# Kernel tuning notes

Measured on AMD Instinct MI355X. Metric: run time of the kernel, lower is better.

The kernel has to match this reference:

```python
import jax, jax.numpy as jnp
import numpy as np

B, H, W, C = 8, 64, 64, 256
CK = C // 8  # key/query dim of conv_f / conv_g


def setup_inputs() -> dict:
    key = jax.random.key(0)
    ks = jax.random.split(key, 10)
    s = lambda fan_in: 1.0 / np.sqrt(fan_in)
    return {
        "x": jax.random.normal(ks[0], (B, H, W, C), dtype=jnp.float32),
        "Wf": jax.random.normal(ks[1], (C, CK), dtype=jnp.float32) * s(C),
        "bf": jnp.zeros((CK,), dtype=jnp.float32),
        "Wg": jax.random.normal(ks[2], (C, CK), dtype=jnp.float32) * s(C),
        "bg": jnp.zeros((CK,), dtype=jnp.float32),
        "Wh": jax.random.normal(ks[3], (C, C), dtype=jnp.float32) * s(C),
        "bh": jnp.zeros((C,), dtype=jnp.float32),
        "Wo": jax.random.normal(ks[4], (C, C), dtype=jnp.float32) * s(C),
        "bo": jnp.zeros((C,), dtype=jnp.float32),
        # original init is zeros; use a random scalar so output/grads are nontrivial
        "gamma": jax.random.normal(ks[5], (1,), dtype=jnp.float32),
    }


def reference(x, Wf, bf, Wg, bg, Wh, bh, Wo, bo, gamma):
    b, h, w, c = x.shape
    n = h * w
    xf = x.reshape(b, n, c)                       # flatten spatial: [B, N, C]
    # 1x1 convs == per-pixel matmuls
    f = xf @ Wf + bf                              # [B, N, C//8]
    g = xf @ Wg + bg                              # [B, N, C//8]
    hh = xf @ Wh + bh                             # [B, N, C]
    # scores[b, i, j] = <g_i, f_j>; softmax over j (keys)
    scores = jnp.einsum("bnd,bmd->bnm", g, f)     # [B, N, N]
    attn = jax.nn.softmax(scores, axis=-1)
    o = jnp.einsum("bnm,bmc->bnc", attn, hh)      # [B, N, C]
    o = o @ Wo + bo                               # conv_o (1x1)
    out = gamma * o + xf                          # gamma residual
    return out.reshape(b, h, w, c)
```

## Files before the change

kernel.cpp:

```cpp
#include <hip/hip_runtime.h>
#include <hip/hip_fp16.h>
#include <hip/hip_bf16.h>

constexpr int BB  = 8;
constexpr int NN  = 4096;
constexpr int CC  = 256;
constexpr int CKK = 32;

typedef __attribute__((ext_vector_type(8))) short    short8;
typedef __attribute__((ext_vector_type(8))) _Float16 half8;
typedef __attribute__((ext_vector_type(4))) _Float16 half4;
typedef __attribute__((ext_vector_type(4))) float    f32x4;

__device__ __forceinline__ unsigned short bf16_bits(float v) {
    __hip_bfloat16 h = __float2bfloat16(v);
    return *reinterpret_cast<unsigned short*>(&h);
}
__device__ __forceinline__ float bf16_val(unsigned short u) {
    __hip_bfloat16 h = *reinterpret_cast<__hip_bfloat16*>(&u);
    return __bfloat162float(h);
}
__device__ __forceinline__ float exp2_x(float x) {
#if __has_builtin(__builtin_amdgcn_exp2f)
    return __builtin_amdgcn_exp2f(x);
#else
    return exp2f(x);
#endif
}

__global__ __launch_bounds__(256) void prep_kernel(
    const float* __restrict__ Wf, const float* __restrict__ Wg,
    const float* __restrict__ Wh, const float* __restrict__ Wo,
    unsigned short* __restrict__ WThi, unsigned short* __restrict__ WTlo)
{
    const int n = blockIdx.x;
    const int k = threadIdx.x;
    float v;
    if      (n < 256) v = Wh[k * 256 + n];
    else if (n < 288) v = Wf[k * 32 + (n - 256)];
    else if (n < 320) v = Wg[k * 32 + (n - 288)];
    else              v = Wo[k * 256 + (n - 320)];
    const unsigned short hi = bf16_bits(v);
    WThi[n * 256 + k] = hi;
    WTlo[n * 256 + k] = bf16_bits(v - bf16_val(hi));
}

__global__ __launch_bounds__(256) void fgh_kernel(
    const float* __restrict__ x,
    const unsigned short* __restrict__ WThi, const unsigned short* __restrict__ WTlo,
    const float* __restrict__ bf, const float* __restrict__ bg,
    const float* __restrict__ bh,
    _Float16* __restrict__ fbuf, _Float16* __restrict__ gbuf,
    _Float16* __restrict__ hhT)
{
    __shared__ __align__(16) float XT[2][64 * 36];

    const int tid = threadIdx.x, w = tid >> 6, lane = tid & 63;
    const int ln = lane & 15, lq = lane >> 4;
    const int b  = blockIdx.x & 7;
    const int q0 = (blockIdx.x >> 3) * 64;
    const size_t px0 = (size_t)b * NN + q0;
    const int n0 = w * 80;

    const int p  = tid >> 2;
    const int jq = tid & 3;
    const float* xrow = &x[(px0 + p) * CC + jq * 8];

    f32x4 acc[4][5];
    #pragma unroll
    for (int i = 0; i < 4; ++i)
        #pragma unroll
        for (int j = 0; j < 5; ++j) acc[i][j] = {0.f, 0.f, 0.f, 0.f};

    short8 Ahi[4], Alo[4];
    float4 ra0 = *(const float4*)&xrow[0];
    float4 ra1 = *(const float4*)&xrow[4];

    int cur = 0;
    #pragma unroll 1
    for (int kc = 0; kc < 8; ++kc) {
        const int k0 = kc * 32;
        float* dst = &XT[cur][p * 36 + jq * 8];
        *(float4*)&dst[0] = ra0;
        *(float4*)&dst[4] = ra1;
        __syncthreads();
        if (kc < 7) {
            ra0 = *(const float4*)&xrow[(kc + 1) * 32];
            ra1 = *(const float4*)&xrow[(kc + 1) * 32 + 4];
        }
        #pragma unroll
        for (int mt = 0; mt < 4; ++mt) {
            float av[8];
            const float* sp = &XT[cur][(mt * 16 + ln) * 36 + lq * 8];
            *(float4*)&av[0] = *(const float4*)&sp[0];
            *(float4*)&av[4] = *(const float4*)&sp[4];
            #pragma unroll
            for (int j = 0; j < 8; ++j) {
                const unsigned short h = bf16_bits(av[j]);
                Ahi[mt][j] = (short)h;
                Alo[mt][j] = (short)bf16_bits(av[j] - bf16_val(h));
            }
        }
        #pragma unroll
        for (int nt = 0; nt < 5; ++nt) {
            const size_t boff = (size_t)(n0 + nt * 16 + ln) * 256 + k0 + lq * 8;
            const short8 Bhi = *(const short8*)&WThi[boff];
            const short8 Blo = *(const short8*)&WTlo[boff];
            #pragma unroll
            for (int mt = 0; mt < 4; ++mt) {
                acc[mt][nt] = __builtin_amdgcn_mfma_f32_16x16x32_bf16(Ahi[mt], Bhi, acc[mt][nt], 0, 0, 0);
                acc[mt][nt] = __builtin_amdgcn_mfma_f32_16x16x32_bf16(Ahi[mt], Blo, acc[mt][nt], 0, 0, 0);
                acc[mt][nt] = __builtin_amdgcn_mfma_f32_16x16x32_bf16(Alo[mt], Bhi, acc[mt][nt], 0, 0, 0);
            }
        }
        cur ^= 1;
    }

    _Float16* st = (_Float16*)&XT[0][0] + w * 1088;
    const int rr = lane >> 3, k8 = lane & 7;

    #pragma unroll
    for (int nt = 0; nt < 5; ++nt) {
        const int cbase = n0 + nt * 16;
        const int c = cbase + ln;
        if (cbase < 256) {
            const float bias = bh[c];
            #pragma unroll
            for (int mt = 0; mt < 4; ++mt) {
                half4 hv;
                #pragma unroll
                for (int r = 0; r < 4; ++r) hv[r] = (_Float16)(acc[mt][nt][r] + bias);
                *(half4*)&st[ln * 68 + mt * 16 + lq * 4] = hv;
            }
            #pragma unroll
            for (int i = 0; i < 2; ++i) {
                const half8 row = *(const half8*)&st[(i * 8 + rr) * 68 + k8 * 8];
                *(half8*)&hhT[((size_t)(b * CC + cbase + i * 8 + rr)) * NN + q0 + k8 * 8] = row;
            }
        } else {
            const bool isf = (c < 288);
            const int d = isf ? (c - 256) : (c - 288);
            const float bias = isf ? bf[d] : bg[d];
            _Float16* dst2 = isf ? fbuf : gbuf;
            #pragma unroll
            for (int mt = 0; mt < 4; ++mt)
                #pragma unroll
                for (int r = 0; r < 4; ++r)
                    dst2[(px0 + mt * 16 + lq * 4 + r) * CKK + d] =
                        (_Float16)(acc[mt][nt][r] + bias);
        }
    }
}

__global__ __launch_bounds__(256) void rowmax_kernel(
    const _Float16* __restrict__ fbuf, const _Float16* __restrict__ gbuf,
    float* __restrict__ mxpart)
{
    __shared__ float mxbuf[4][64];

    const int tid = threadIdx.x, w = tid >> 6, lane = tid & 63;
    const int ln = lane & 15, lq = lane >> 4;
    const int b  = blockIdx.x & 7;
    const int q0 = (blockIdx.x >> 3) * 64;
    const int kp = blockIdx.y;

    const f32x4 zero = {0.f, 0.f, 0.f, 0.f};

    half8 Bg[4];
    #pragma unroll
    for (int qt = 0; qt < 4; ++qt)
        Bg[qt] = *(const half8*)&gbuf[(size_t)(b * NN + q0 + qt * 16 + ln) * CKK + lq * 8];

    const _Float16* fb = &fbuf[(size_t)(b * NN + kp * 1024 + w * 16 + ln) * CKK + lq * 8];

    float mx[4];
    #pragma unroll
    for (int qt = 0; qt < 4; ++qt) mx[qt] = -1e30f;
    half8 Afc = *(const half8*)fb;
    #pragma unroll 1
    for (int j0 = 0; j0 < 1024; j0 += 64) {
        const int jn = (j0 + 64 < 1024) ? j0 + 64 : j0;
        const half8 Afn = *(const half8*)&fb[(size_t)jn * CKK];
        #pragma unroll
        for (int qt = 0; qt < 4; ++qt) {
            const f32x4 s = __builtin_amdgcn_mfma_f32_16x16x32_f16(Afc, Bg[qt], zero, 0, 0, 0);
            mx[qt] = fmaxf(mx[qt], fmaxf(fmaxf(s[0], s[1]), fmaxf(s[2], s[3])));
        }
        Afc = Afn;
    }
    #pragma unroll
    for (int qt = 0; qt < 4; ++qt) {
        mx[qt] = fmaxf(mx[qt], __shfl_xor(mx[qt], 16));
        mx[qt] = fmaxf(mx[qt], __shfl_xor(mx[qt], 32));
    }
    if (lane < 16) {
        #pragma unroll
        for (int qt = 0; qt < 4; ++qt) mxbuf[w][qt * 16 + ln] = mx[qt];
    }
    __syncthreads();
    if (tid < 64) {
        const float m = fmaxf(fmaxf(mxbuf[0][tid], mxbuf[1][tid]),
                              fmaxf(mxbuf[2][tid], mxbuf[3][tid]));
        mxpart[(size_t)kp * (BB * NN) + (size_t)b * NN + q0 + tid] = m;
    }
}

__global__ __launch_bounds__(256, 2) void attn_kernel(
    const _Float16* __restrict__ fbuf, const _Float16* __restrict__ gbuf,
    const _Float16* __restrict__ hhT, const float* __restrict__ mxpart,
    const unsigned short* __restrict__ WThi, const unsigned short* __restrict__ WTlo,
    const float* __restrict__ bo, const float* __restrict__ gamma,
    const float* __restrict__ x, float* __restrict__ out)
{
    __shared__ __align__(16) float OF[64 * 268];
    _Float16* P0 = (_Float16*)OF;
    _Float16* P1 = P0 + 64 * 72;
    __shared__ float rsbuf[4][64];

    const int tid = threadIdx.x, w = tid >> 6, lane = tid & 63;
    const int ln = lane & 15, lq = lane >> 4;
    const int b  = blockIdx.x & 7;
    const int q0 = (blockIdx.x >> 3) * 64;
    const int cb = w * 64;

    const f32x4 zero = {0.f, 0.f, 0.f, 0.f};
    constexpr float LOG2E = 1.4426950408889634f;

    half8 Bg[4];
    #pragma unroll
    for (int qt = 0; qt < 4; ++qt)
        Bg[qt] = *(const half8*)&gbuf[(size_t)(b * NN + q0 + qt * 16 + ln) * CKK + lq * 8];

    const _Float16* fb = &fbuf[(size_t)(b * NN + w * 16 + ln) * CKK + lq * 8];
    const _Float16* hb = &hhT[((size_t)(b * CC + cb + ln)) * NN + lq * 8];

    float mk[4];
    #pragma unroll
    for (int qt = 0; qt < 4; ++qt) {
        const float* mp = &mxpart[(size_t)b * NN + q0 + qt * 16 + ln];
        const float m = fmaxf(fmaxf(mp[0], mp[BB * NN]),
                              fmaxf(mp[2 * (BB * NN)], mp[3 * (BB * NN)]));
        mk[qt] = LOG2E * m;
    }

    f32x4 O[4][4];
    #pragma unroll
    for (int qt = 0; qt < 4; ++qt)
        #pragma unroll
        for (int ct = 0; ct < 4; ++ct) O[qt][ct] = zero;
    float psum[4] = {0.f, 0.f, 0.f, 0.f};

    auto phaseA = [&](const half8& Af, _Float16* Pb) {
        #pragma unroll
        for (int qt = 0; qt < 4; ++qt) {
            const f32x4 s = __builtin_amdgcn_mfma_f32_16x16x32_f16(Af, Bg[qt], zero, 0, 0, 0);
            half4 ph;
            float ps = 0.f;
            #pragma unroll
            for (int r = 0; r < 4; ++r) {
                const float p = exp2_x(fmaf(s[r], LOG2E, -mk[qt]));
                ps += p;
                ph[r] = (_Float16)p;
            }
            psum[qt] += ps;
            *(half4*)&Pb[(qt * 16 + ln) * 72 + w * 16 + lq * 4] = ph;
        }
    };

    auto loadBh = [&](half8 (&Bh)[4][2], int j0) {
        #pragma unroll
        for (int ct = 0; ct < 4; ++ct)
            #pragma unroll
            for (int kh = 0; kh < 2; ++kh)
                Bh[ct][kh] = *(const half8*)&hb[(size_t)ct * 16 * NN + j0 + kh * 32];
    };

    auto phaseB = [&](const half8 (&Bh)[4][2], const _Float16* Pb) {
        __builtin_amdgcn_s_setprio(1);
        #pragma unroll
        for (int qt = 0; qt < 4; ++qt) {
            const half8 Ap0 = *(const half8*)&Pb[(qt * 16 + ln) * 72 + lq * 8];
            const half8 Ap1 = *(const half8*)&Pb[(qt * 16 + ln) * 72 + 32 + lq * 8];
            #pragma unroll
            for (int ct = 0; ct < 4; ++ct) {
                O[qt][ct] = __builtin_amdgcn_mfma_f32_16x16x32_f16(Ap0, Bh[ct][0], O[qt][ct], 0, 0, 0);
                O[qt][ct] = __builtin_amdgcn_mfma_f32_16x16x32_f16(Ap1, Bh[ct][1], O[qt][ct], 0, 0, 0);
            }
        }
        __builtin_amdgcn_s_setprio(0);
    };

    half8 Bh0[4][2], Bh1[4][2];
    half8 Af0, Af1;
    loadBh(Bh0, 0);
    Af0 = *(const half8*)fb;

    #pragma unroll 1
    for (int j0 = 0; j0 < NN; j0 += 128) {
        phaseA(Af0, P0);
        __syncthreads();
        loadBh(Bh1, j0 + 64);
        Af1 = *(const half8*)&fb[(size_t)(j0 + 64) * CKK];
        phaseB(Bh0, P0);
        phaseA(Af1, P1);
        __syncthreads();
        if (j0 + 128 < NN) {
            loadBh(Bh0, j0 + 128);
            Af0 = *(const half8*)&fb[(size_t)(j0 + 128) * CKK];
        }
        phaseB(Bh1, P1);
    }

    #pragma unroll
    for (int qt = 0; qt < 4; ++qt) {
        psum[qt] += __shfl_xor(psum[qt], 16);
        psum[qt] += __shfl_xor(psum[qt], 32);
    }
    if (lane < 16) {
        #pragma unroll
        for (int qt = 0; qt < 4; ++qt) rsbuf[w][qt * 16 + ln] = psum[qt];
    }
    __syncthreads();

    #pragma unroll
    for (int qt = 0; qt < 4; ++qt)
        #pragma unroll
        for (int r = 0; r < 4; ++r) {
            const int q = qt * 16 + lq * 4 + r;
            const float rinv = 1.0f / (rsbuf[0][q] + rsbuf[1][q] + rsbuf[2][q] + rsbuf[3][q]);
            #pragma unroll
            for (int ct = 0; ct < 4; ++ct)
                OF[q * 268 + cb + ct * 16 + ln] = O[qt][ct][r] * rinv;
        }
    __syncthreads();

    {
        const int n0 = w * 64;
        f32x4 acc[4][4];
        #pragma unroll
        for (int i = 0; i < 4; ++i)
            #pragma unroll
            for (int j = 0; j < 4; ++j) acc[i][j] = {0.f, 0.f, 0.f, 0.f};

        short8 Ahi[4], Alo[4];
        #pragma unroll 1
        for (int kc = 0; kc < 8; ++kc) {
            const int k0 = kc * 32;
            #pragma unroll
            for (int mt = 0; mt < 4; ++mt) {
                float av[8];
                *(f32x4*)&av[0] = *(const f32x4*)&OF[(mt * 16 + ln) * 268 + k0 + lq * 8];
                *(f32x4*)&av[4] = *(const f32x4*)&OF[(mt * 16 + ln) * 268 + k0 + lq * 8 + 4];
                #pragma unroll
                for (int j = 0; j < 8; ++j) {
                    const unsigned short h = bf16_bits(av[j]);
                    Ahi[mt][j] = (short)h;
                    Alo[mt][j] = (short)bf16_bits(av[j] - bf16_val(h));
                }
            }
            #pragma unroll
            for (int nt = 0; nt < 4; ++nt) {
                const size_t boff = (size_t)(320 + n0 + nt * 16 + ln) * 256 + k0 + lq * 8;
                const short8 Bhi = *(const short8*)&WThi[boff];
                const short8 Blo = *(const short8*)&WTlo[boff];
                #pragma unroll
                for (int mt = 0; mt < 4; ++mt) {
                    acc[mt][nt] = __builtin_amdgcn_mfma_f32_16x16x32_bf16(Ahi[mt], Bhi, acc[mt][nt], 0, 0, 0);
                    acc[mt][nt] = __builtin_amdgcn_mfma_f32_16x16x32_bf16(Ahi[mt], Blo, acc[mt][nt], 0, 0, 0);
                    acc[mt][nt] = __builtin_amdgcn_mfma_f32_16x16x32_bf16(Alo[mt], Bhi, acc[mt][nt], 0, 0, 0);
                }
            }
        }

        const float gm = gamma[0];
        #pragma unroll
        for (int nt = 0; nt < 4; ++nt) {
            const int c = n0 + nt * 16 + ln;
            const float bias = bo[c];
            #pragma unroll
            for (int mt = 0; mt < 4; ++mt)
                #pragma unroll
                for (int r = 0; r < 4; ++r) {
                    const size_t idx = (size_t)(b * NN + q0 + mt * 16 + lq * 4 + r) * CC + c;
                    out[idx] = gm * (acc[mt][nt][r] + bias) + x[idx];
                }
        }
    }
}

extern "C" void kernel_launch(void* const* d_in, const int* in_sizes, int n_in,
                              void* d_out, int out_size, void* d_ws, size_t ws_size,
                              hipStream_t stream)
{
    (void)in_sizes; (void)n_in; (void)out_size; (void)ws_size;

    const float* x     = (const float*)d_in[0];
    const float* Wf    = (const float*)d_in[1];
    const float* bf    = (const float*)d_in[2];
    const float* Wg    = (const float*)d_in[3];
    const float* bg    = (const float*)d_in[4];
    const float* Wh    = (const float*)d_in[5];
    const float* bh    = (const float*)d_in[6];
    const float* Wo    = (const float*)d_in[7];
    const float* bo    = (const float*)d_in[8];
    const float* gamma = (const float*)d_in[9];
    float* out = (float*)d_out;

    _Float16* fbuf = (_Float16*)d_ws;
    _Float16* gbuf = fbuf + (size_t)BB * NN * CKK;
    _Float16* hhT  = gbuf + (size_t)BB * NN * CKK;
    unsigned short* WThi = (unsigned short*)(hhT + (size_t)BB * CC * NN);
    unsigned short* WTlo = WThi + (size_t)576 * 256;
    float* mxpart = (float*)(WTlo + (size_t)576 * 256);

    prep_kernel<<<576, 256, 0, stream>>>(Wf, Wg, Wh, Wo, WThi, WTlo);
    fgh_kernel<<<BB * NN / 64, 256, 0, stream>>>(x, WThi, WTlo, bf, bg, bh,
                                                 fbuf, gbuf, hhT);
    rowmax_kernel<<<dim3(BB * NN / 64, 4), 256, 0, stream>>>(fbuf, gbuf, mxpart);
    attn_kernel<<<BB * NN / 64, 256, 0, stream>>>(fbuf, gbuf, hhT, mxpart, WThi, WTlo,
                                                  bo, gamma, x, out);
}
```

Before: 282.2 us.

## Deepen attention pipeline to four P buffers and split rowmax over eight key chunks

```diff
diff --git a/kernel.cpp b/kernel.cpp
--- a/kernel.cpp
+++ b/kernel.cpp
@@ -171,15 +171,15 @@
     for (int qt = 0; qt < 4; ++qt)
         Bg[qt] = *(const half8*)&gbuf[(size_t)(b * NN + q0 + qt * 16 + ln) * CKK + lq * 8];
 
-    const _Float16* fb = &fbuf[(size_t)(b * NN + kp * 1024 + w * 16 + ln) * CKK + lq * 8];
+    const _Float16* fb = &fbuf[(size_t)(b * NN + kp * 512 + w * 16 + ln) * CKK + lq * 8];
 
     float mx[4];
     #pragma unroll
     for (int qt = 0; qt < 4; ++qt) mx[qt] = -1e30f;
     half8 Afc = *(const half8*)fb;
     #pragma unroll 1
-    for (int j0 = 0; j0 < 1024; j0 += 64) {
-        const int jn = (j0 + 64 < 1024) ? j0 + 64 : j0;
+    for (int j0 = 0; j0 < 512; j0 += 64) {
+        const int jn = (j0 + 64 < 512) ? j0 + 64 : j0;
         const half8 Afn = *(const half8*)&fb[(size_t)jn * CKK];
         #pragma unroll
         for (int qt = 0; qt < 4; ++qt) {
@@ -205,7 +205,7 @@
     }
 }
 
-__global__ __launch_bounds__(256, 2) void attn_kernel(
+__global__ __launch_bounds__(256, 1) void attn_kernel(
     const _Float16* __restrict__ fbuf, const _Float16* __restrict__ gbuf,
     const _Float16* __restrict__ hhT, const float* __restrict__ mxpart,
     const unsigned short* __restrict__ WThi, const unsigned short* __restrict__ WTlo,
@@ -213,8 +213,9 @@
     const float* __restrict__ x, float* __restrict__ out)
 {
     __shared__ __align__(16) float OF[64 * 268];
-    _Float16* P0 = (_Float16*)OF;
-    _Float16* P1 = P0 + 64 * 72;
+    _Float16* Pq[4];
+    #pragma unroll
+    for (int i = 0; i < 4; ++i) Pq[i] = (_Float16*)OF + i * 64 * 72;
     __shared__ float rsbuf[4][64];
 
     const int tid = threadIdx.x, w = tid >> 6, lane = tid & 63;
@@ -238,8 +239,9 @@
     #pragma unroll
     for (int qt = 0; qt < 4; ++qt) {
         const float* mp = &mxpart[(size_t)b * NN + q0 + qt * 16 + ln];
-        const float m = fmaxf(fmaxf(mp[0], mp[BB * NN]),
-                              fmaxf(mp[2 * (BB * NN)], mp[3 * (BB * NN)]));
+        float m = mp[0];
+        #pragma unroll
+        for (int pp = 1; pp < 8; ++pp) m = fmaxf(m, mp[(size_t)pp * (BB * NN)]);
         mk[qt] = LOG2E * m;
     }
 
@@ -291,24 +293,37 @@
     };
 
     half8 Bh0[4][2], Bh1[4][2];
-    half8 Af0, Af1;
     loadBh(Bh0, 0);
-    Af0 = *(const half8*)fb;
+    loadBh(Bh1, 64);
+    half8 Af0 = *(const half8*)fb;
+    half8 Af1 = *(const half8*)&fb[(size_t)64 * CKK];
+    phaseA(Af0, Pq[0]);
+    phaseA(Af1, Pq[1]);
+    Af0 = *(const half8*)&fb[(size_t)128 * CKK];
+    Af1 = *(const half8*)&fb[(size_t)192 * CKK];
 
     #pragma unroll 1
-    for (int j0 = 0; j0 < NN; j0 += 128) {
-        phaseA(Af0, P0);
+    for (int j0 = 0; j0 < NN; j0 += 256) {
         __syncthreads();
-        loadBh(Bh1, j0 + 64);
-        Af1 = *(const half8*)&fb[(size_t)(j0 + 64) * CKK];
-        phaseB(Bh0, P0);
-        phaseA(Af1, P1);
+        phaseB(Bh0, Pq[0]);
+        loadBh(Bh0, j0 + 128);
+        phaseB(Bh1, Pq[1]);
+        loadBh(Bh1, j0 + 192);
+        phaseA(Af0, Pq[2]);
+        Af0 = *(const half8*)&fb[(size_t)((j0 + 256) & (NN - 1)) * CKK];
+        phaseA(Af1, Pq[3]);
+        Af1 = *(const half8*)&fb[(size_t)((j0 + 320) & (NN - 1)) * CKK];
         __syncthreads();
-        if (j0 + 128 < NN) {
-            loadBh(Bh0, j0 + 128);
-            Af0 = *(const half8*)&fb[(size_t)(j0 + 128) * CKK];
-        }
-        phaseB(Bh1, P1);
+        phaseB(Bh0, Pq[2]);
+        phaseB(Bh1, Pq[3]);
+        if (j0 + 256 < NN) {
+            loadBh(Bh0, j0 + 256);
+            loadBh(Bh1, j0 + 320);
+            phaseA(Af0, Pq[0]);
+            Af0 = *(const half8*)&fb[(size_t)((j0 + 384) & (NN - 1)) * CKK];
+            phaseA(Af1, Pq[1]);
+            Af1 = *(const half8*)&fb[(size_t)((j0 + 448) & (NN - 1)) * CKK];
+        }
     }
 
     #pragma unroll
@@ -416,7 +431,7 @@
     prep_kernel<<<576, 256, 0, stream>>>(Wf, Wg, Wh, Wo, WThi, WTlo);
     fgh_kernel<<<BB * NN / 64, 256, 0, stream>>>(x, WThi, WTlo, bf, bg, bh,
                                                  fbuf, gbuf, hhT);
-    rowmax_kernel<<<dim3(BB * NN / 64, 4), 256, 0, stream>>>(fbuf, gbuf, mxpart);
+    rowmax_kernel<<<dim3(BB * NN / 64, 8), 256, 0, stream>>>(fbuf, gbuf, mxpart);
     attn_kernel<<<BB * NN / 64, 256, 0, stream>>>(fbuf, gbuf, hhT, mxpart, WThi, WTlo,
                                                   bo, gamma, x, out);
 }
```

Result: slower. 297.2 us (+5.3%).
